# Kernel optimization log

Measured on AMD Instinct MI355X. Metric: run time of the kernel, lower is better.

Reference implementation:

```python
import jax, jax.numpy as jnp
import numpy as np

C = 1024
H = 16
EPS = 1e-5

def layernorm(x, g, b):
    mu = jnp.mean(x, axis=-1, keepdims=True)
    var = jnp.var(x, axis=-1, keepdims=True)
    return (x - mu) * jax.lax.rsqrt(var + EPS) * g + b

def setup_inputs() -> dict:
    key = jax.random.key(0)
    ks = jax.random.split(key, 12)
    s = lambda fan: 1.0 / np.sqrt(fan)
    return {
        "x": jax.random.normal(ks[0], (2, 2048, C), jnp.float32),
        "W_qkv": jax.random.uniform(ks[1], (C, 3 * C), jnp.float32, -s(C), s(C)),
        "W_o": jax.random.uniform(ks[2], (C, C), jnp.float32, -s(C), s(C)),
        "b_o": jnp.zeros((C,), jnp.float32),
        "g1": jnp.ones((C,), jnp.float32),
        "beta1": jnp.zeros((C,), jnp.float32),
        "g2": jnp.ones((C,), jnp.float32),
        "beta2": jnp.zeros((C,), jnp.float32),
        "W_ff1": jax.random.uniform(ks[3], (C, 4 * C), jnp.float32, -s(C), s(C)),
        "b_ff1": jnp.zeros((4 * C,), jnp.float32),
        "W_ff2": jax.random.uniform(ks[4], (4 * C, C), jnp.float32, -s(4 * C), s(4 * C)),
        "b_ff2": jnp.zeros((C,), jnp.float32),
    }

def reference(x, W_qkv, W_o, b_o, g1, beta1, g2, beta2, W_ff1, b_ff1, W_ff2, b_ff2):
    B, T, _ = x.shape
    hd = C // H  # head dim
    # --- self-attention on norm1(x) ---
    h = layernorm(x, g1, beta1)
    qkv = h @ W_qkv                      # [B,T,3C]
    q, k, v = jnp.split(qkv, 3, axis=-1)
    reshp = lambda t: t.reshape(B, T, H, hd).transpose(0, 2, 1, 3)  # [B,H,T,hd]
    q, k, v = reshp(q), reshp(k), reshp(v)
    att = jnp.einsum("bhqd,bhkd->bhqk", q, k) * (hd ** -0.5)
    causal = jnp.tril(jnp.ones((T, T), bool))
    att = jnp.where(causal, att, -jnp.inf)
    att = jax.nn.softmax(att, axis=-1)
    out = jnp.einsum("bhqk,bhkd->bhqd", att, v)
    out = out.transpose(0, 2, 1, 3).reshape(B, T, C)
    x = x + out @ W_o + b_o
    # --- feed-forward on norm2(x) ---
    h = layernorm(x, g2, beta2)
    h = jax.nn.relu(h @ W_ff1 + b_ff1) @ W_ff2 + b_ff2
    return x + h
```

## Files before the change

### kernel.cpp

```cpp
#include <hip/hip_runtime.h>
#include <hip/hip_bf16.h>
#include <stdint.h>


typedef __attribute__((ext_vector_type(8))) short bf16x8;
typedef __attribute__((ext_vector_type(4))) float f32x4;

#define MFMA16(a, b, c) __builtin_amdgcn_mfma_f32_16x16x32_bf16((a), (b), (c), 0, 0, 0)

__device__ __forceinline__ void gload16(const void* g, void* l) {
    __builtin_amdgcn_global_load_lds(
        (const __attribute__((address_space(1))) char*)g,
        (__attribute__((address_space(3))) char*)l, 16, 0, 0);
}

__device__ __forceinline__ int xcd_swizzle(int flat, int nblk) {
    if ((nblk & 7) == 0) {
        const int per = nblk >> 3;
        flat = (flat & 7) * per + (flat >> 3);
    }
    return flat;
}

__global__ __launch_bounds__(256) void tconv_all(
    const float* __restrict__ w0, __hip_bfloat16* __restrict__ o0,
    const float* __restrict__ w1, __hip_bfloat16* __restrict__ o1,
    const float* __restrict__ w2, __hip_bfloat16* __restrict__ o2,
    const float* __restrict__ w3, __hip_bfloat16* __restrict__ o3) {
    __shared__ float tile[32][33];
    const int f = blockIdx.x;
    const float* in; __hip_bfloat16* out; int K, N, nx, t;
    if (f < 3072)      { in = w0; out = o0; K = 1024; N = 3072; nx = 96;  t = f; }
    else if (f < 4096) { in = w1; out = o1; K = 1024; N = 1024; nx = 32;  t = f - 3072; }
    else if (f < 8192) { in = w2; out = o2; K = 1024; N = 4096; nx = 128; t = f - 4096; }
    else               { in = w3; out = o3; K = 4096; N = 1024; nx = 32;  t = f - 8192; }
    const int n0 = (t % nx) * 32, k0 = (t / nx) * 32;
    const int tx = threadIdx.x, ty = threadIdx.y;
    for (int i = ty; i < 32; i += 8)
        tile[i][tx] = in[(size_t)(k0 + i) * N + n0 + tx];
    __syncthreads();
    for (int i = ty; i < 32; i += 8)
        out[(size_t)(n0 + i) * K + k0 + tx] = __float2bfloat16(tile[tx][i]);
}

__global__ __launch_bounds__(256) void ln_k(const float* __restrict__ x,
                                            const float* __restrict__ g,
                                            const float* __restrict__ beta,
                                            __hip_bfloat16* __restrict__ out) {
    const int row = blockIdx.x;
    const int tid = threadIdx.x;
    float4 v = ((const float4*)(x + (size_t)row * 1024))[tid];
    float s  = v.x + v.y + v.z + v.w;
    float s2 = v.x * v.x + v.y * v.y + v.z * v.z + v.w * v.w;
    for (int off = 1; off < 64; off <<= 1) {
        s  += __shfl_xor(s,  off, 64);
        s2 += __shfl_xor(s2, off, 64);
    }
    __shared__ float ss[4], ss2[4];
    const int w = tid >> 6, lane = tid & 63;
    if (lane == 0) { ss[w] = s; ss2[w] = s2; }
    __syncthreads();
    s  = ss[0] + ss[1] + ss[2] + ss[3];
    s2 = ss2[0] + ss2[1] + ss2[2] + ss2[3];
    const float mu  = s * (1.0f / 1024.0f);
    const float var = s2 * (1.0f / 1024.0f) - mu * mu;
    const float rs  = rsqrtf(var + 1e-5f);
    float4 gv = ((const float4*)g)[tid];
    float4 bv = ((const float4*)beta)[tid];
    __hip_bfloat16* o = out + (size_t)row * 1024 + tid * 4;
    o[0] = __float2bfloat16((v.x - mu) * rs * gv.x + bv.x);
    o[1] = __float2bfloat16((v.y - mu) * rs * gv.y + bv.y);
    o[2] = __float2bfloat16((v.z - mu) * rs * gv.z + bv.z);
    o[3] = __float2bfloat16((v.w - mu) * rs * gv.w + bv.w);
}

template <int BIAS, int RELU, int RESID, int OUTBF>
__global__ __launch_bounds__(256, 2) void gemm_k(const __hip_bfloat16* __restrict__ A,
                                                 const __hip_bfloat16* __restrict__ Bt,
                                                 const float* __restrict__ bias,
                                                 const float* __restrict__ resid,
                                                 void* __restrict__ out,
                                                 int M, int N, int K) {
    __align__(16) __shared__ __hip_bfloat16 As[2][128 * 64];
    __align__(16) __shared__ __hip_bfloat16 Bs[2][128 * 64];

    const int tid  = threadIdx.x;
    const int lane = tid & 63, w = tid >> 6;
    const int wm = w >> 1, wn = w & 1;
    const int nbx = gridDim.x;
    const int flat = xcd_swizzle(blockIdx.y * nbx + blockIdx.x, nbx * gridDim.y);
    const int m0 = (flat / nbx) * 128, n0 = (flat % nbx) * 128;
    const int l16 = lane & 15, quad = lane >> 4;

    const int srw = lane >> 3;
    const int scn = ((lane & 7) - srw) & 7;

    const __hip_bfloat16* ga[4];
    const __hip_bfloat16* gb[4];
#pragma unroll
    for (int i = 0; i < 4; i++) {
        const int row = i * 32 + w * 8 + srw;
        ga[i] = A  + (size_t)(m0 + row) * K + scn * 8;
        gb[i] = Bt + (size_t)(n0 + row) * K + scn * 8;
    }

    int offA[2][4], offB[2][4];
#pragma unroll
    for (int s = 0; s < 2; s++)
#pragma unroll
        for (int t = 0; t < 4; t++) {
            const int rA = wm * 64 + t * 16 + l16;
            offA[s][t] = (rA * 8 + ((s * 4 + quad + (rA & 7)) & 7)) * 16;
            const int rB = wn * 64 + t * 16 + l16;
            offB[s][t] = (rB * 8 + ((s * 4 + quad + (rB & 7)) & 7)) * 16;
        }

    f32x4 acc[4][4] = {};

#pragma unroll
    for (int i = 0; i < 4; i++) {
        gload16(ga[i], As[0] + (i * 256 + w * 64) * 8);
        gload16(gb[i], Bs[0] + (i * 256 + w * 64) * 8);
        ga[i] += 64; gb[i] += 64;
    }

    const int niter = K >> 6;
    for (int it = 0; it < niter; it++) {
        const int buf = it & 1;
        __syncthreads();
        if (it + 1 < niter) {
#pragma unroll
            for (int i = 0; i < 4; i++) {
                gload16(ga[i], As[buf ^ 1] + (i * 256 + w * 64) * 8);
                gload16(gb[i], Bs[buf ^ 1] + (i * 256 + w * 64) * 8);
                ga[i] += 64; gb[i] += 64;
            }
        }

#pragma unroll
        for (int s = 0; s < 2; s++) {
            bf16x8 af[4], bfr[4];
#pragma unroll
            for (int t = 0; t < 4; t++) {
                af[t]  = *(const bf16x8*)((const char*)As[buf] + offA[s][t]);
                bfr[t] = *(const bf16x8*)((const char*)Bs[buf] + offB[s][t]);
            }
#pragma unroll
            for (int mt = 0; mt < 4; mt++)
#pragma unroll
                for (int nt = 0; nt < 4; nt++)
                    acc[mt][nt] = MFMA16(af[mt], bfr[nt], acc[mt][nt]);
        }
    }

#pragma unroll
    for (int mt = 0; mt < 4; mt++)
#pragma unroll
        for (int nt = 0; nt < 4; nt++) {
            const int row = m0 + wm * 64 + mt * 16 + quad * 4;
            const int col = n0 + wn * 64 + nt * 16 + l16;
            const float bv = BIAS ? bias[col] : 0.0f;
#pragma unroll
            for (int r = 0; r < 4; r++) {
                float v = acc[mt][nt][r] + bv;
                if (RELU) v = v > 0.0f ? v : 0.0f;
                const size_t idx = (size_t)(row + r) * N + col;
                if (RESID) v += resid[idx];
                if (OUTBF) ((__hip_bfloat16*)out)[idx] = __float2bfloat16(v);
                else       ((float*)out)[idx] = v;
            }
        }
}

template <int BIAS, int RELU, int RESID, int OUTBF>
__global__ __launch_bounds__(256, 4) void gemm6464_k(const __hip_bfloat16* __restrict__ A,
                                                     const __hip_bfloat16* __restrict__ Bt,
                                                     const float* __restrict__ bias,
                                                     const float* __restrict__ resid,
                                                     void* __restrict__ out,
                                                     int M, int N, int K) {
    __align__(16) __shared__ __hip_bfloat16 As[2][64 * 64];
    __align__(16) __shared__ __hip_bfloat16 Bs[2][64 * 64];

    const int tid  = threadIdx.x;
    const int lane = tid & 63, w = tid >> 6;
    const int wm = w >> 1, wn = w & 1;
    const int nbx = gridDim.x;
    const int flat = xcd_swizzle(blockIdx.y * nbx + blockIdx.x, nbx * gridDim.y);
    const int m0 = (flat / nbx) * 64, n0 = (flat % nbx) * 64;
    const int l16 = lane & 15, quad = lane >> 4;

    const int srw = lane >> 3;
    const int scn = ((lane & 7) - srw) & 7;

    const __hip_bfloat16* ga[2];
    const __hip_bfloat16* gb[2];
#pragma unroll
    for (int i = 0; i < 2; i++) {
        const int row = i * 32 + w * 8 + srw;
        ga[i] = A  + (size_t)(m0 + row) * K + scn * 8;
        gb[i] = Bt + (size_t)(n0 + row) * K + scn * 8;
    }

    int offA[2][2], offB[2][2];
#pragma unroll
    for (int s = 0; s < 2; s++)
#pragma unroll
        for (int t = 0; t < 2; t++) {
            const int rA = wm * 32 + t * 16 + l16;
            offA[s][t] = (rA * 8 + ((s * 4 + quad + (rA & 7)) & 7)) * 16;
            const int rB = wn * 32 + t * 16 + l16;
            offB[s][t] = (rB * 8 + ((s * 4 + quad + (rB & 7)) & 7)) * 16;
        }

    f32x4 acc[2][2] = {};

#pragma unroll
    for (int i = 0; i < 2; i++) {
        gload16(ga[i], As[0] + (i * 256 + w * 64) * 8);
        gload16(gb[i], Bs[0] + (i * 256 + w * 64) * 8);
        ga[i] += 64; gb[i] += 64;
    }

    const int niter = K >> 6;
    for (int it = 0; it < niter; it++) {
        const int buf = it & 1;
        __syncthreads();
        if (it + 1 < niter) {
#pragma unroll
            for (int i = 0; i < 2; i++) {
                gload16(ga[i], As[buf ^ 1] + (i * 256 + w * 64) * 8);
                gload16(gb[i], Bs[buf ^ 1] + (i * 256 + w * 64) * 8);
                ga[i] += 64; gb[i] += 64;
            }
        }

#pragma unroll
        for (int s = 0; s < 2; s++) {
            bf16x8 af[2], bfr[2];
#pragma unroll
            for (int t = 0; t < 2; t++) {
                af[t]  = *(const bf16x8*)((const char*)As[buf] + offA[s][t]);
                bfr[t] = *(const bf16x8*)((const char*)Bs[buf] + offB[s][t]);
            }
#pragma unroll
            for (int mt = 0; mt < 2; mt++)
#pragma unroll
                for (int nt = 0; nt < 2; nt++)
                    acc[mt][nt] = MFMA16(af[mt], bfr[nt], acc[mt][nt]);
        }
    }

#pragma unroll
    for (int mt = 0; mt < 2; mt++)
#pragma unroll
        for (int nt = 0; nt < 2; nt++) {
            const int row = m0 + wm * 32 + mt * 16 + quad * 4;
            const int col = n0 + wn * 32 + nt * 16 + l16;
            const float bv = BIAS ? bias[col] : 0.0f;
#pragma unroll
            for (int r = 0; r < 4; r++) {
                float v = acc[mt][nt][r] + bv;
                if (RELU) v = v > 0.0f ? v : 0.0f;
                const size_t idx = (size_t)(row + r) * N + col;
                if (RESID) v += resid[idx];
                if (OUTBF) ((__hip_bfloat16*)out)[idx] = __float2bfloat16(v);
                else       ((float*)out)[idx] = v;
            }
        }
}

__global__ __launch_bounds__(256) void vtrans_k(const __hip_bfloat16* __restrict__ qkv,
                                                __hip_bfloat16* __restrict__ vt) {
    const int T = 2048, C3 = 3072;
    const int bh = blockIdx.y, b = bh >> 4, h = bh & 15;
    const int t0 = blockIdx.x * 64;
    const int tx = threadIdx.x, ty = threadIdx.y;
    __shared__ __hip_bfloat16 tile[64][65];
#pragma unroll
    for (int j = 0; j < 16; j++) {
        const int tl = ty * 16 + j;
        tile[tl][tx] = qkv[(size_t)(b * T + t0 + tl) * C3 + 2048 + h * 64 + tx];
    }
    __syncthreads();
#pragma unroll
    for (int j = 0; j < 16; j++) {
        const int d = ty * 16 + j;
        vt[((size_t)bh * 64 + d) * 2048 + t0 + tx] = tile[tx][d];
    }
}

__global__ __launch_bounds__(256, 3) void attn_k(const __hip_bfloat16* __restrict__ qkv,
                                                 const __hip_bfloat16* __restrict__ vt,
                                                 __hip_bfloat16* __restrict__ outp) {
    const int T = 2048, C3 = 3072;
    const int bh = blockIdx.x, b = bh >> 4, h = bh & 15;
    const int qt = 31 - blockIdx.y;
    const int q0 = qt * 64;
    const int tid = threadIdx.x, lane = tid & 63, w = tid >> 6;
    const int l16 = lane & 15, quad = lane >> 4;

    __align__(16) __shared__ __hip_bfloat16 Ks[2][64 * 64];
    __align__(16) __shared__ __hip_bfloat16 Vs[2][64 * 64];
    __align__(16) __shared__ __hip_bfloat16 Pw[4][16 * 72];

    const float sc = 0.125f * 1.44269504f;
    bf16x8 qf0, qf1;
    {
        const __hip_bfloat16* qp =
            qkv + (size_t)(b * T + q0 + w * 16 + l16) * C3 + h * 64;
        bf16x8 a = *(const bf16x8*)(qp + quad * 8);
        bf16x8 c = *(const bf16x8*)(qp + 32 + quad * 8);
#pragma unroll
        for (int i = 0; i < 8; i++) {
            union { unsigned int u; float f; } ua, uc;
            ua.u = ((unsigned int)(unsigned short)a[i]) << 16;
            uc.u = ((unsigned int)(unsigned short)c[i]) << 16;
            qf0[i] = (short)(__bfloat16_as_ushort(__float2bfloat16(ua.f * sc)));
            qf1[i] = (short)(__bfloat16_as_ushort(__float2bfloat16(uc.f * sc)));
        }
    }

    const int srw = lane >> 3;
    const int scn = ((lane & 7) - srw) & 7;
    const __hip_bfloat16* kp[2];
    const __hip_bfloat16* vp[2];
#pragma unroll
    for (int i = 0; i < 2; i++) {
        const int row = i * 32 + w * 8 + srw;
        kp[i] = qkv + (size_t)(b * T + row) * C3 + 1024 + h * 64 + scn * 8;
        vp[i] = vt + ((size_t)bh * 64 + row) * 2048 + scn * 8;
    }

    int offK[2][4];
#pragma unroll
    for (int s = 0; s < 2; s++)
#pragma unroll
        for (int t = 0; t < 4; t++) {
            const int rr = t * 16 + l16;
            offK[s][t] = (rr * 8 + ((s * 4 + quad + (rr & 7)) & 7)) * 16;
        }

    f32x4 oacc[4] = {};
    float lpart[4] = {0.0f, 0.0f, 0.0f, 0.0f};

#pragma unroll
    for (int i = 0; i < 2; i++) {
        gload16(kp[i], Ks[0] + (i * 256 + w * 64) * 8);
        gload16(vp[i], Vs[0] + (i * 256 + w * 64) * 8);
    }

    for (int kt = 0; kt <= qt; kt++) {
        const int buf = kt & 1;
        __syncthreads();
        if (kt < qt) {
#pragma unroll
            for (int i = 0; i < 2; i++) {
                gload16(kp[i] + (size_t)(kt + 1) * 64 * C3,
                        Ks[buf ^ 1] + (i * 256 + w * 64) * 8);
                gload16(vp[i] + (kt + 1) * 64,
                        Vs[buf ^ 1] + (i * 256 + w * 64) * 8);
            }
        }

        f32x4 s4[4];
#pragma unroll
        for (int nt = 0; nt < 4; nt++) {
            bf16x8 kf0 = *(const bf16x8*)((const char*)Ks[buf] + offK[0][nt]);
            bf16x8 kf1 = *(const bf16x8*)((const char*)Ks[buf] + offK[1][nt]);
            f32x4 z = {};
            z = MFMA16(qf0, kf0, z);
            z = MFMA16(qf1, kf1, z);
            s4[nt] = z;
        }

        const bool diag = (kt == qt);
        const int myrow = w * 16 + quad * 4;
#pragma unroll
        for (int nt = 0; nt < 4; nt++) {
            const int col = nt * 16 + l16;
#pragma unroll
            for (int r = 0; r < 4; r++) {
                float p = exp2f(s4[nt][r]);
                if (diag && col > myrow + r) p = 0.0f;
                lpart[r] += p;
                Pw[w][(quad * 4 + r) * 72 + col] = __float2bfloat16(p);
            }
        }

        asm volatile("s_waitcnt lgkmcnt(0)" ::: "memory");

        bf16x8 pf0 = *(const bf16x8*)(&Pw[w][l16 * 72 + quad * 8]);
        bf16x8 pf1 = *(const bf16x8*)(&Pw[w][l16 * 72 + 32 + quad * 8]);
#pragma unroll
        for (int dt = 0; dt < 4; dt++) {
            bf16x8 vf0 = *(const bf16x8*)((const char*)Vs[buf] + offK[0][dt]);
            bf16x8 vf1 = *(const bf16x8*)((const char*)Vs[buf] + offK[1][dt]);
            oacc[dt] = MFMA16(pf0, vf0, oacc[dt]);
            oacc[dt] = MFMA16(pf1, vf1, oacc[dt]);
        }
    }

#pragma unroll
    for (int off = 1; off < 16; off <<= 1)
#pragma unroll
        for (int r = 0; r < 4; r++)
            lpart[r] += __shfl_xor(lpart[r], off, 64);

    float rl[4];
#pragma unroll
    for (int r = 0; r < 4; r++) rl[r] = 1.0f / lpart[r];
#pragma unroll
    for (int dt = 0; dt < 4; dt++)
#pragma unroll
        for (int r = 0; r < 4; r++) {
            const int row = q0 + w * 16 + quad * 4 + r;
            outp[(size_t)(b * T + row) * 1024 + h * 64 + dt * 16 + l16] =
                __float2bfloat16(oacc[dt][r] * rl[r]);
        }
}

extern "C" void kernel_launch(void* const* d_in, const int* in_sizes, int n_in,
                              void* d_out, int out_size, void* d_ws, size_t ws_size,
                              hipStream_t stream) {
    const float* x     = (const float*)d_in[0];
    const float* Wqkv  = (const float*)d_in[1];
    const float* Wo    = (const float*)d_in[2];
    const float* b_o   = (const float*)d_in[3];
    const float* g1    = (const float*)d_in[4];
    const float* beta1 = (const float*)d_in[5];
    const float* g2    = (const float*)d_in[6];
    const float* beta2 = (const float*)d_in[7];
    const float* Wff1  = (const float*)d_in[8];
    const float* bff1  = (const float*)d_in[9];
    const float* Wff2  = (const float*)d_in[10];
    const float* bff2  = (const float*)d_in[11];

    char* ws = (char*)d_ws;
    size_t off = 0;
    auto alloc = [&](size_t bytes) {
        void* p = ws + off;
        off += (bytes + 255) & ~(size_t)255;
        return p;
    };
    __hip_bfloat16* Wqkv_t = (__hip_bfloat16*)alloc(3072ULL * 1024 * 2);
    __hip_bfloat16* Wo_t   = (__hip_bfloat16*)alloc(1024ULL * 1024 * 2);
    __hip_bfloat16* Wff1_t = (__hip_bfloat16*)alloc(4096ULL * 1024 * 2);
    __hip_bfloat16* Wff2_t = (__hip_bfloat16*)alloc(1024ULL * 4096 * 2);
    __hip_bfloat16* h_bf   = (__hip_bfloat16*)alloc(4096ULL * 1024 * 2);
    __hip_bfloat16* qkv_bf = (__hip_bfloat16*)alloc(4096ULL * 3072 * 2);
    __hip_bfloat16* att_bf = (__hip_bfloat16*)alloc(4096ULL * 1024 * 2);
    float*          x2     = (float*)alloc(4096ULL * 1024 * 4);
    __hip_bfloat16* ff1_bf = qkv_bf;
    __hip_bfloat16* vt     = (__hip_bfloat16*)x2;

    tconv_all<<<12288, dim3(32, 8), 0, stream>>>(Wqkv, Wqkv_t, Wo, Wo_t,
                                                 Wff1, Wff1_t, Wff2, Wff2_t);

    ln_k<<<4096, 256, 0, stream>>>(x, g1, beta1, h_bf);
    gemm_k<0, 0, 0, 1><<<dim3(3072 / 128, 4096 / 128), 256, 0, stream>>>(
        h_bf, Wqkv_t, nullptr, nullptr, qkv_bf, 4096, 3072, 1024);
    vtrans_k<<<dim3(32, 32), dim3(64, 4), 0, stream>>>(qkv_bf, vt);
    attn_k<<<dim3(32, 32), 256, 0, stream>>>(qkv_bf, vt, att_bf);
    gemm6464_k<1, 0, 1, 0><<<dim3(1024 / 64, 4096 / 64), 256, 0, stream>>>(
        att_bf, Wo_t, b_o, x, x2, 4096, 1024, 1024);
    ln_k<<<4096, 256, 0, stream>>>(x2, g2, beta2, h_bf);
    gemm_k<1, 1, 0, 1><<<dim3(4096 / 128, 4096 / 128), 256, 0, stream>>>(
        h_bf, Wff1_t, bff1, nullptr, ff1_bf, 4096, 4096, 1024);
    gemm6464_k<1, 0, 1, 0><<<dim3(1024 / 64, 4096 / 64), 256, 0, stream>>>(
        ff1_bf, Wff2_t, bff2, x2, (float*)d_out, 4096, 1024, 4096);
}
```

Measured before the change: 325.7 us.

## Use 128x128x32 GEMM tile with higher occupancy and split-K for FF2

Replaces the 128x128x64 GEMM with a 128x128x32 K-step variant that uses half the LDS per block and allows four blocks per CU. It also adds split-K (four partitions) for the FF2 projection, writing fp32 partial sums that a separate reduction kernel adds together with the bias and residual. The smaller K step means more barriers per unit of work. Split-K adds 64MB of partial-sum traffic plus an extra launch in exchange for more parallel blocks and larger tiles on the K=4096 GEMM.

New measurement: 338.7 us. +4.0%, slower.

```diff
diff --git a/kernel.cpp b/kernel.cpp
--- a/kernel.cpp
+++ b/kernel.cpp
@@ -74,15 +74,15 @@
     o[3] = __float2bfloat16((v.w - mu) * rs * gv.w + bv.w);
 }
 
-template <int BIAS, int RELU, int RESID, int OUTBF>
-__global__ __launch_bounds__(256, 2) void gemm_k(const __hip_bfloat16* __restrict__ A,
-                                                 const __hip_bfloat16* __restrict__ Bt,
-                                                 const float* __restrict__ bias,
-                                                 const float* __restrict__ resid,
-                                                 void* __restrict__ out,
-                                                 int M, int N, int K) {
-    __align__(16) __shared__ __hip_bfloat16 As[2][128 * 64];
-    __align__(16) __shared__ __hip_bfloat16 Bs[2][128 * 64];
+template <int BIAS, int RELU, int RESID, int OUTBF, int PART>
+__global__ __launch_bounds__(256, 4) void gemm32_k(const __hip_bfloat16* __restrict__ A,
+                                                   const __hip_bfloat16* __restrict__ Bt,
+                                                   const float* __restrict__ bias,
+                                                   const float* __restrict__ resid,
+                                                   void* __restrict__ out,
+                                                   int M, int N, int K, int kper) {
+    __align__(16) __shared__ __hip_bfloat16 As[2][128 * 32];
+    __align__(16) __shared__ __hip_bfloat16 Bs[2][128 * 32];
 
     const int tid  = threadIdx.x;
     const int lane = tid & 63, w = tid >> 6;
@@ -90,67 +90,65 @@
     const int nbx = gridDim.x;
     const int flat = xcd_swizzle(blockIdx.y * nbx + blockIdx.x, nbx * gridDim.y);
     const int m0 = (flat / nbx) * 128, n0 = (flat % nbx) * 128;
+    const int z  = blockIdx.z;
     const int l16 = lane & 15, quad = lane >> 4;
 
-    const int srw = lane >> 3;
-    const int scn = ((lane & 7) - srw) & 7;
-
-    const __hip_bfloat16* ga[4];
-    const __hip_bfloat16* gb[4];
-#pragma unroll
-    for (int i = 0; i < 4; i++) {
-        const int row = i * 32 + w * 8 + srw;
-        ga[i] = A  + (size_t)(m0 + row) * K + scn * 8;
-        gb[i] = Bt + (size_t)(n0 + row) * K + scn * 8;
-    }
-
-    int offA[2][4], offB[2][4];
-#pragma unroll
-    for (int s = 0; s < 2; s++)
-#pragma unroll
-        for (int t = 0; t < 4; t++) {
-            const int rA = wm * 64 + t * 16 + l16;
-            offA[s][t] = (rA * 8 + ((s * 4 + quad + (rA & 7)) & 7)) * 16;
-            const int rB = wn * 64 + t * 16 + l16;
-            offB[s][t] = (rB * 8 + ((s * 4 + quad + (rB & 7)) & 7)) * 16;
-        }
+    const int srw4 = lane >> 2;
+    const int c4   = lane & 3;
+    const int scn4 = (c4 - (srw4 & 3) - (srw4 >> 2)) & 3;
+
+    const __hip_bfloat16* ga[2];
+    const __hip_bfloat16* gb[2];
+#pragma unroll
+    for (int i = 0; i < 2; i++) {
+        const int row = i * 64 + w * 16 + srw4;
+        ga[i] = A  + (size_t)(m0 + row) * K + (size_t)z * kper + scn4 * 8;
+        gb[i] = Bt + (size_t)(n0 + row) * K + (size_t)z * kper + scn4 * 8;
+    }
+
+    const int rotr = (quad + l16 + (l16 >> 2)) & 3;
+    int offA[4], offB[4];
+#pragma unroll
+    for (int t = 0; t < 4; t++) {
+        const int rA = wm * 64 + t * 16 + l16;
+        offA[t] = rA * 64 + rotr * 16;
+        const int rB = wn * 64 + t * 16 + l16;
+        offB[t] = rB * 64 + rotr * 16;
+    }
 
     f32x4 acc[4][4] = {};
 
 #pragma unroll
-    for (int i = 0; i < 4; i++) {
-        gload16(ga[i], As[0] + (i * 256 + w * 64) * 8);
-        gload16(gb[i], Bs[0] + (i * 256 + w * 64) * 8);
-        ga[i] += 64; gb[i] += 64;
-    }
-
-    const int niter = K >> 6;
+    for (int i = 0; i < 2; i++) {
+        gload16(ga[i], As[0] + (i * 64 + w * 16) * 32);
+        gload16(gb[i], Bs[0] + (i * 64 + w * 16) * 32);
+        ga[i] += 32; gb[i] += 32;
+    }
+
+    const int niter = kper >> 5;
     for (int it = 0; it < niter; it++) {
         const int buf = it & 1;
         __syncthreads();
         if (it + 1 < niter) {
 #pragma unroll
-            for (int i = 0; i < 4; i++) {
-                gload16(ga[i], As[buf ^ 1] + (i * 256 + w * 64) * 8);
-                gload16(gb[i], Bs[buf ^ 1] + (i * 256 + w * 64) * 8);
-                ga[i] += 64; gb[i] += 64;
-            }
-        }
-
-#pragma unroll
-        for (int s = 0; s < 2; s++) {
-            bf16x8 af[4], bfr[4];
-#pragma unroll
-            for (int t = 0; t < 4; t++) {
-                af[t]  = *(const bf16x8*)((const char*)As[buf] + offA[s][t]);
-                bfr[t] = *(const bf16x8*)((const char*)Bs[buf] + offB[s][t]);
-            }
-#pragma unroll
-            for (int mt = 0; mt < 4; mt++)
-#pragma unroll
-                for (int nt = 0; nt < 4; nt++)
-                    acc[mt][nt] = MFMA16(af[mt], bfr[nt], acc[mt][nt]);
-        }
+            for (int i = 0; i < 2; i++) {
+                gload16(ga[i], As[buf ^ 1] + (i * 64 + w * 16) * 32);
+                gload16(gb[i], Bs[buf ^ 1] + (i * 64 + w * 16) * 32);
+                ga[i] += 32; gb[i] += 32;
+            }
+        }
+
+        bf16x8 af[4], bfr[4];
+#pragma unroll
+        for (int t = 0; t < 4; t++) {
+            af[t]  = *(const bf16x8*)((const char*)As[buf] + offA[t]);
+            bfr[t] = *(const bf16x8*)((const char*)Bs[buf] + offB[t]);
+        }
+#pragma unroll
+        for (int mt = 0; mt < 4; mt++)
+#pragma unroll
+            for (int nt = 0; nt < 4; nt++)
+                acc[mt][nt] = MFMA16(af[mt], bfr[nt], acc[mt][nt]);
     }
 
 #pragma unroll
@@ -165,11 +163,35 @@
                 float v = acc[mt][nt][r] + bv;
                 if (RELU) v = v > 0.0f ? v : 0.0f;
                 const size_t idx = (size_t)(row + r) * N + col;
-                if (RESID) v += resid[idx];
-                if (OUTBF) ((__hip_bfloat16*)out)[idx] = __float2bfloat16(v);
-                else       ((float*)out)[idx] = v;
-            }
-        }
+                if (PART) {
+                    ((float*)out)[(size_t)z * M * N + idx] = v;
+                } else {
+                    if (RESID) v += resid[idx];
+                    if (OUTBF) ((__hip_bfloat16*)out)[idx] = __float2bfloat16(v);
+                    else       ((float*)out)[idx] = v;
+                }
+            }
+        }
+}
+
+__global__ __launch_bounds__(256) void reduce4_k(const float* __restrict__ parts,
+                                                 const float* __restrict__ bias,
+                                                 const float* __restrict__ resid,
+                                                 float* __restrict__ out) {
+    const size_t f = (size_t)blockIdx.x * 256 + threadIdx.x;
+    const size_t STRIDE = 4096ULL * 1024 / 4;
+    float4 a = ((const float4*)parts)[f];
+    float4 b = ((const float4*)parts)[f + STRIDE];
+    float4 c = ((const float4*)parts)[f + 2 * STRIDE];
+    float4 d = ((const float4*)parts)[f + 3 * STRIDE];
+    float4 rv = ((const float4*)resid)[f];
+    float4 bv = ((const float4*)bias)[f & 255];
+    float4 o;
+    o.x = a.x + b.x + c.x + d.x + rv.x + bv.x;
+    o.y = a.y + b.y + c.y + d.y + rv.y + bv.y;
+    o.z = a.z + b.z + c.z + d.z + rv.z + bv.z;
+    o.w = a.w + b.w + c.w + d.w + rv.w + bv.w;
+    ((float4*)out)[f] = o;
 }
 
 template <int BIAS, int RELU, int RESID, int OUTBF>
@@ -451,6 +473,7 @@
     __hip_bfloat16* qkv_bf = (__hip_bfloat16*)alloc(4096ULL * 3072 * 2);
     __hip_bfloat16* att_bf = (__hip_bfloat16*)alloc(4096ULL * 1024 * 2);
     float*          x2     = (float*)alloc(4096ULL * 1024 * 4);
+    float*          parts  = (float*)alloc(4ULL * 4096 * 1024 * 4);
     __hip_bfloat16* ff1_bf = qkv_bf;
     __hip_bfloat16* vt     = (__hip_bfloat16*)x2;
 
@@ -458,15 +481,16 @@
                                                  Wff1, Wff1_t, Wff2, Wff2_t);
 
     ln_k<<<4096, 256, 0, stream>>>(x, g1, beta1, h_bf);
-    gemm_k<0, 0, 0, 1><<<dim3(3072 / 128, 4096 / 128), 256, 0, stream>>>(
-        h_bf, Wqkv_t, nullptr, nullptr, qkv_bf, 4096, 3072, 1024);
+    gemm32_k<0, 0, 0, 1, 0><<<dim3(3072 / 128, 4096 / 128, 1), 256, 0, stream>>>(
+        h_bf, Wqkv_t, nullptr, nullptr, qkv_bf, 4096, 3072, 1024, 1024);
     vtrans_k<<<dim3(32, 32), dim3(64, 4), 0, stream>>>(qkv_bf, vt);
     attn_k<<<dim3(32, 32), 256, 0, stream>>>(qkv_bf, vt, att_bf);
     gemm6464_k<1, 0, 1, 0><<<dim3(1024 / 64, 4096 / 64), 256, 0, stream>>>(
         att_bf, Wo_t, b_o, x, x2, 4096, 1024, 1024);
     ln_k<<<4096, 256, 0, stream>>>(x2, g2, beta2, h_bf);
-    gemm_k<1, 1, 0, 1><<<dim3(4096 / 128, 4096 / 128), 256, 0, stream>>>(
-        h_bf, Wff1_t, bff1, nullptr, ff1_bf, 4096, 4096, 1024);
-    gemm6464_k<1, 0, 1, 0><<<dim3(1024 / 64, 4096 / 64), 256, 0, stream>>>(
-        ff1_bf, Wff2_t, bff2, x2, (float*)d_out, 4096, 1024, 4096);
-}
+    gemm32_k<1, 1, 0, 1, 0><<<dim3(4096 / 128, 4096 / 128, 1), 256, 0, stream>>>(
+        h_bf, Wff1_t, bff1, nullptr, ff1_bf, 4096, 4096, 1024, 1024);
+    gemm32_k<0, 0, 0, 0, 1><<<dim3(1024 / 128, 4096 / 128, 4), 256, 0, stream>>>(
+        ff1_bf, Wff2_t, nullptr, nullptr, parts, 4096, 1024, 4096, 1024);
+    reduce4_k<<<4096, 256, 0, stream>>>(parts, bff2, x2, (float*)d_out);
+}
```

## Load A fragments directly from global into registers in 64x64 GEMM

Applied to the files above, without the earlier changes.

The 64x64 GEMM used for the output projection and FF2 no longer stages the A tile through LDS. Each wave loads its A MFMA fragments straight from global memory into registers, double-buffered across an unrolled pair of K iterations, while B stays in LDS. This cuts LDS traffic and LDS footprint in exchange for redundant global A reads: both N-waves read the same rows, and the per-lane 16-byte loads are strided by row. It also raises register pressure and assumes an even number of K iterations.

Result: slower. 436.6 us (+34.1%).

```diff
diff --git a/kernel.cpp b/kernel.cpp
--- a/kernel.cpp
+++ b/kernel.cpp
@@ -173,13 +173,12 @@
 }
 
 template <int BIAS, int RELU, int RESID, int OUTBF>
-__global__ __launch_bounds__(256, 4) void gemm6464_k(const __hip_bfloat16* __restrict__ A,
-                                                     const __hip_bfloat16* __restrict__ Bt,
-                                                     const float* __restrict__ bias,
-                                                     const float* __restrict__ resid,
-                                                     void* __restrict__ out,
-                                                     int M, int N, int K) {
-    __align__(16) __shared__ __hip_bfloat16 As[2][64 * 64];
+__global__ __launch_bounds__(256, 4) void gemm_flat_k(const __hip_bfloat16* __restrict__ A,
+                                                      const __hip_bfloat16* __restrict__ Bt,
+                                                      const float* __restrict__ bias,
+                                                      const float* __restrict__ resid,
+                                                      void* __restrict__ out,
+                                                      int M, int N, int K) {
     __align__(16) __shared__ __hip_bfloat16 Bs[2][64 * 64];
 
     const int tid  = threadIdx.x;
@@ -193,61 +192,93 @@
     const int srw = lane >> 3;
     const int scn = ((lane & 7) - srw) & 7;
 
-    const __hip_bfloat16* ga[2];
     const __hip_bfloat16* gb[2];
 #pragma unroll
     for (int i = 0; i < 2; i++) {
         const int row = i * 32 + w * 8 + srw;
-        ga[i] = A  + (size_t)(m0 + row) * K + scn * 8;
         gb[i] = Bt + (size_t)(n0 + row) * K + scn * 8;
     }
 
-    int offA[2][2], offB[2][2];
+    int offB[2][2];
 #pragma unroll
     for (int s = 0; s < 2; s++)
 #pragma unroll
         for (int t = 0; t < 2; t++) {
-            const int rA = wm * 32 + t * 16 + l16;
-            offA[s][t] = (rA * 8 + ((s * 4 + quad + (rA & 7)) & 7)) * 16;
             const int rB = wn * 32 + t * 16 + l16;
             offB[s][t] = (rB * 8 + ((s * 4 + quad + (rB & 7)) & 7)) * 16;
         }
 
+    const __hip_bfloat16* pA = A + (size_t)(m0 + wm * 32 + l16) * K + quad * 8;
+
     f32x4 acc[2][2] = {};
+    bf16x8 afa[2][2], afb[2][2];
 
 #pragma unroll
     for (int i = 0; i < 2; i++) {
-        gload16(ga[i], As[0] + (i * 256 + w * 64) * 8);
         gload16(gb[i], Bs[0] + (i * 256 + w * 64) * 8);
-        ga[i] += 64; gb[i] += 64;
-    }
+        gb[i] += 64;
+    }
+#pragma unroll
+    for (int s = 0; s < 2; s++)
+#pragma unroll
+        for (int t = 0; t < 2; t++)
+            afa[s][t] = *(const bf16x8*)(pA + (size_t)(t * 16) * K + s * 32);
+    pA += 64;
 
     const int niter = K >> 6;
-    for (int it = 0; it < niter; it++) {
-        const int buf = it & 1;
+    for (int it = 0; it < niter; it += 2) {
         __syncthreads();
-        if (it + 1 < niter) {
+#pragma unroll
+        for (int i = 0; i < 2; i++) {
+            gload16(gb[i], Bs[1] + (i * 256 + w * 64) * 8);
+            gb[i] += 64;
+        }
+#pragma unroll
+        for (int s = 0; s < 2; s++)
+#pragma unroll
+            for (int t = 0; t < 2; t++)
+                afb[s][t] = *(const bf16x8*)(pA + (size_t)(t * 16) * K + s * 32);
+        pA += 64;
+
+#pragma unroll
+        for (int s = 0; s < 2; s++) {
+            bf16x8 bfr[2];
+#pragma unroll
+            for (int t = 0; t < 2; t++)
+                bfr[t] = *(const bf16x8*)((const char*)Bs[0] + offB[s][t]);
+#pragma unroll
+            for (int mt = 0; mt < 2; mt++)
+#pragma unroll
+                for (int nt = 0; nt < 2; nt++)
+                    acc[mt][nt] = MFMA16(afa[s][mt], bfr[nt], acc[mt][nt]);
+        }
+
+        __syncthreads();
+        if (it + 2 < niter) {
 #pragma unroll
             for (int i = 0; i < 2; i++) {
-                gload16(ga[i], As[buf ^ 1] + (i * 256 + w * 64) * 8);
-                gload16(gb[i], Bs[buf ^ 1] + (i * 256 + w * 64) * 8);
-                ga[i] += 64; gb[i] += 64;
-            }
+                gload16(gb[i], Bs[0] + (i * 256 + w * 64) * 8);
+                gb[i] += 64;
+            }
+#pragma unroll
+            for (int s = 0; s < 2; s++)
+#pragma unroll
+                for (int t = 0; t < 2; t++)
+                    afa[s][t] = *(const bf16x8*)(pA + (size_t)(t * 16) * K + s * 32);
+            pA += 64;
         }
 
 #pragma unroll
         for (int s = 0; s < 2; s++) {
-            bf16x8 af[2], bfr[2];
-#pragma unroll
-            for (int t = 0; t < 2; t++) {
-                af[t]  = *(const bf16x8*)((const char*)As[buf] + offA[s][t]);
-                bfr[t] = *(const bf16x8*)((const char*)Bs[buf] + offB[s][t]);
-            }
+            bf16x8 bfr[2];
+#pragma unroll
+            for (int t = 0; t < 2; t++)
+                bfr[t] = *(const bf16x8*)((const char*)Bs[1] + offB[s][t]);
 #pragma unroll
             for (int mt = 0; mt < 2; mt++)
 #pragma unroll
                 for (int nt = 0; nt < 2; nt++)
-                    acc[mt][nt] = MFMA16(af[mt], bfr[nt], acc[mt][nt]);
+                    acc[mt][nt] = MFMA16(afb[s][mt], bfr[nt], acc[mt][nt]);
         }
     }
 
@@ -462,11 +493,11 @@
         h_bf, Wqkv_t, nullptr, nullptr, qkv_bf, 4096, 3072, 1024);
     vtrans_k<<<dim3(32, 32), dim3(64, 4), 0, stream>>>(qkv_bf, vt);
     attn_k<<<dim3(32, 32), 256, 0, stream>>>(qkv_bf, vt, att_bf);
-    gemm6464_k<1, 0, 1, 0><<<dim3(1024 / 64, 4096 / 64), 256, 0, stream>>>(
+    gemm_flat_k<1, 0, 1, 0><<<dim3(1024 / 64, 4096 / 64), 256, 0, stream>>>(
         att_bf, Wo_t, b_o, x, x2, 4096, 1024, 1024);
     ln_k<<<4096, 256, 0, stream>>>(x2, g2, beta2, h_bf);
     gemm_k<1, 1, 0, 1><<<dim3(4096 / 128, 4096 / 128), 256, 0, stream>>>(
         h_bf, Wff1_t, bff1, nullptr, ff1_bf, 4096, 4096, 1024);
-    gemm6464_k<1, 0, 1, 0><<<dim3(1024 / 64, 4096 / 64), 256, 0, stream>>>(
+    gemm_flat_k<1, 0, 1, 0><<<dim3(1024 / 64, 4096 / 64), 256, 0, stream>>>(
         ff1_bf, Wff2_t, bff2, x2, (float*)d_out, 4096, 1024, 4096);
 }
```

## Triple-buffer 64x64 GEMM shared memory with vmcnt-gated barriers

Applied to the files above, without the earlier changes.

Converts the 64x64 GEMM kernel from double to triple LDS buffering, prefetching two K-tiles ahead. Each phase waits on vmcnt to retire only the oldest tile's loads before a raw s_barrier, so global loads stay in flight across iterations. This costs more LDS per block, and occupancy is lowered from 4 to 3 blocks per CU to match.

Result: slower. 362.5 us (+11.3%).

```diff
diff --git a/kernel.cpp b/kernel.cpp
--- a/kernel.cpp
+++ b/kernel.cpp
@@ -173,14 +173,14 @@
 }
 
 template <int BIAS, int RELU, int RESID, int OUTBF>
-__global__ __launch_bounds__(256, 4) void gemm6464_k(const __hip_bfloat16* __restrict__ A,
+__global__ __launch_bounds__(256, 3) void gemm6464_k(const __hip_bfloat16* __restrict__ A,
                                                      const __hip_bfloat16* __restrict__ Bt,
                                                      const float* __restrict__ bias,
                                                      const float* __restrict__ resid,
                                                      void* __restrict__ out,
                                                      int M, int N, int K) {
-    __align__(16) __shared__ __hip_bfloat16 As[2][64 * 64];
-    __align__(16) __shared__ __hip_bfloat16 Bs[2][64 * 64];
+    __align__(16) __shared__ __hip_bfloat16 As[3][64 * 64];
+    __align__(16) __shared__ __hip_bfloat16 Bs[3][64 * 64];
 
     const int tid  = threadIdx.x;
     const int lane = tid & 63, w = tid >> 6;
@@ -215,41 +215,57 @@
 
     f32x4 acc[2][2] = {};
 
+    const int niter = K >> 6;
+
 #pragma unroll
     for (int i = 0; i < 2; i++) {
         gload16(ga[i], As[0] + (i * 256 + w * 64) * 8);
         gload16(gb[i], Bs[0] + (i * 256 + w * 64) * 8);
         ga[i] += 64; gb[i] += 64;
     }
-
-    const int niter = K >> 6;
-    for (int it = 0; it < niter; it++) {
-        const int buf = it & 1;
-        __syncthreads();
-        if (it + 1 < niter) {
-#pragma unroll
-            for (int i = 0; i < 2; i++) {
-                gload16(ga[i], As[buf ^ 1] + (i * 256 + w * 64) * 8);
-                gload16(gb[i], Bs[buf ^ 1] + (i * 256 + w * 64) * 8);
-                ga[i] += 64; gb[i] += 64;
-            }
-        }
-
-#pragma unroll
-        for (int s = 0; s < 2; s++) {
-            bf16x8 af[2], bfr[2];
-#pragma unroll
-            for (int t = 0; t < 2; t++) {
-                af[t]  = *(const bf16x8*)((const char*)As[buf] + offA[s][t]);
-                bfr[t] = *(const bf16x8*)((const char*)Bs[buf] + offB[s][t]);
-            }
-#pragma unroll
-            for (int mt = 0; mt < 2; mt++)
-#pragma unroll
-                for (int nt = 0; nt < 2; nt++)
-                    acc[mt][nt] = MFMA16(af[mt], bfr[nt], acc[mt][nt]);
-        }
-    }
+#pragma unroll
+    for (int i = 0; i < 2; i++) {
+        gload16(ga[i], As[1] + (i * 256 + w * 64) * 8);
+        gload16(gb[i], Bs[1] + (i * 256 + w * 64) * 8);
+        ga[i] += 64; gb[i] += 64;
+    }
+
+#define GPHASE(T, BUF, PRE)                                                   \
+    do {                                                                      \
+        if ((T) + 1 < niter) asm volatile("s_waitcnt vmcnt(4)" ::: "memory"); \
+        else                 asm volatile("s_waitcnt vmcnt(0)" ::: "memory"); \
+        __builtin_amdgcn_s_barrier();                                         \
+        asm volatile("" ::: "memory");                                        \
+        if ((T) + 2 < niter) {                                                \
+            _Pragma("unroll")                                                 \
+            for (int i = 0; i < 2; i++) {                                     \
+                gload16(ga[i], As[PRE] + (i * 256 + w * 64) * 8);             \
+                gload16(gb[i], Bs[PRE] + (i * 256 + w * 64) * 8);             \
+                ga[i] += 64; gb[i] += 64;                                     \
+            }                                                                 \
+        }                                                                     \
+        _Pragma("unroll")                                                     \
+        for (int s = 0; s < 2; s++) {                                         \
+            bf16x8 af[2], bfr[2];                                             \
+            _Pragma("unroll")                                                 \
+            for (int t = 0; t < 2; t++) {                                     \
+                af[t]  = *(const bf16x8*)((const char*)As[BUF] + offA[s][t]); \
+                bfr[t] = *(const bf16x8*)((const char*)Bs[BUF] + offB[s][t]); \
+            }                                                                 \
+            _Pragma("unroll")                                                 \
+            for (int mt = 0; mt < 2; mt++)                                    \
+                _Pragma("unroll")                                             \
+                for (int nt = 0; nt < 2; nt++)                                \
+                    acc[mt][nt] = MFMA16(af[mt], bfr[nt], acc[mt][nt]);       \
+        }                                                                     \
+    } while (0)
+
+    for (int t3 = 0; t3 < niter; t3 += 3) {
+        GPHASE(t3, 0, 2);
+        if (t3 + 1 < niter) GPHASE(t3 + 1, 1, 0);
+        if (t3 + 2 < niter) GPHASE(t3 + 2, 2, 1);
+    }
+#undef GPHASE
 
 #pragma unroll
     for (int mt = 0; mt < 2; mt++)
```
